# Optimization experiments

Measured on AMD Instinct MI355X. Metric: run time of the kernel, lower is better.

Reference implementation:

```python
import jax, jax.numpy as jnp
import numpy as np

TEMP = 0.07
EPS = 1e-8
NUM_CLASSES = 7
THRESH = 0.3


def setup_inputs() -> dict:
    key = jax.random.key(0)
    k1, k2, k3, k4, k5 = jax.random.split(key, 5)
    N, H, E, C = 8192, 128, 256, NUM_CLASSES
    reps = jax.random.normal(k1, (N, H), dtype=jnp.float32)
    labels = jax.random.randint(k2, (N,), 0, C, dtype=jnp.int64 if jax.config.jax_enable_x64 else jnp.int32)
    centers = jax.random.normal(k3, (C, E), dtype=jnp.float32)
    fc_w = jax.random.normal(k4, (H, E), dtype=jnp.float32) * (1.0 / np.sqrt(E))
    fc_b = jax.random.normal(k5, (H,), dtype=jnp.float32) * 0.01
    return {"reps": reps, "labels": labels, "centers": centers, "fc_w": fc_w, "fc_b": fc_b}


def reference(reps, labels, centers, fc_w, fc_b):
    # fc(default_centers): [C, H]
    curr_centers = centers @ fc_w.T + fc_b
    pad_labels = jnp.arange(NUM_CLASSES, dtype=labels.dtype)

    all_reps = jnp.concatenate([reps, curr_centers], axis=0)      # [M, H]
    all_labels = jnp.concatenate([labels, pad_labels], axis=0)    # [M]
    B = reps.shape[0]
    M = all_reps.shape[0]

    # cosine similarity via normalized matmul (avoids [B,M,H] broadcast)
    norms = jnp.sqrt(jnp.sum(all_reps * all_reps, axis=-1))
    rn = all_reps / jnp.maximum(norms, 1e-8)[:, None]
    cos = rn[:B] @ rn.T                                           # [B, M]

    scores = (1.0 + cos) * 0.5 + EPS
    eye = (jnp.arange(B)[:, None] == jnp.arange(M)[None, :]).astype(scores.dtype)
    scores = scores * (1.0 - eye) / TEMP
    # torch uses .item() on the max -> a non-differentiable constant
    scores = scores - jax.lax.stop_gradient(jnp.max(scores))
    e = jnp.exp(scores)

    pos_mask = (labels[:, None] == all_labels[None, :]).astype(scores.dtype)  # [B, M]
    mask = 1.0 - eye

    pos_sum = jnp.sum(e * pos_mask * mask, axis=-1)
    neg_sum = jnp.sum(e * (1.0 - pos_mask), axis=-1)
    probs = pos_sum / (pos_sum + neg_sum)
    probs = probs / (jnp.sum(pos_mask * mask, axis=-1) + EPS)

    loss_vec = -jnp.log(probs + EPS)
    loss_mask = (loss_vec > THRESH).astype(loss_vec.dtype)
    denom = jax.lax.stop_gradient(jnp.sum(loss_mask)) + EPS
    loss = jnp.sum(loss_vec * loss_mask) / denom
    return loss
```

## Files before the change

### kernel.cpp

```cpp
#include <hip/hip_runtime.h>
#include <hip/hip_bf16.h>

#define BN 8192
#define MM 8199
#define MP 8208
#define HH 128
#define EE 256
#define GX 128
#define GY 16
#define NUM_HIST 7

typedef __attribute__((ext_vector_type(8))) short short8;
typedef __attribute__((ext_vector_type(4))) float floatx4;


__global__ __launch_bounds__(256)
void prep_kernel(const float* __restrict__ reps,
                 const int* __restrict__ labels,
                 const float* __restrict__ centers,
                 const float* __restrict__ fc_w,
                 const float* __restrict__ fc_b,
                 __hip_bfloat16* __restrict__ rnt,
                 int* __restrict__ labp,
                 float* __restrict__ tot) {
  const int wid = threadIdx.x >> 6, lane = threadIdx.x & 63;
  const int b = blockIdx.x;
  if (b < 2048) {
    if (threadIdx.x < 8) tot[b * 8 + threadIdx.x] = 0.f;
    const int r = b * 4 + wid;
    float2 v = ((const float2*)(reps + (size_t)r * HH))[lane];
    float ss = v.x * v.x + v.y * v.y;
#pragma unroll
    for (int m = 1; m < 64; m <<= 1) ss += __shfl_xor(ss, m);
    float inv = 1.0f / fmaxf(sqrtf(ss), 1e-8f);
    __hip_bfloat162 h2;
    h2.x = __float2bfloat16(v.x * inv);
    h2.y = __float2bfloat16(v.y * inv);
    size_t o = (size_t)(r >> 4) * 1024 + (lane >> 2) * 64 + (r & 15) * 4 + (lane & 3);
    ((__hip_bfloat162*)rnt)[o] = h2;
    if (lane == 0) labp[r] = labels[r];
  } else {
    __shared__ float currs[7 * HH];
    for (int o = threadIdx.x; o < 7 * HH; o += 256) {
      int c = o >> 7, h = o & 127;
      const float4* ce = (const float4*)(centers + c * EE);
      const float4* w  = (const float4*)(fc_w + h * EE);
      float s = 0.f;
#pragma unroll 4
      for (int j = 0; j < EE / 4; ++j) {
        float4 a = ce[j], bb = w[j];
        s += a.x * bb.x + a.y * bb.y + a.z * bb.z + a.w * bb.w;
      }
      currs[o] = s + fc_b[h];
    }
    __syncthreads();
    for (int k = 0; k < 4; ++k) {
      int c = wid * 4 + k;
      int r = BN + c;
      float2 v = make_float2(0.f, 0.f);
      if (c < 7) v = ((const float2*)(currs + c * HH))[lane];
      float ss = v.x * v.x + v.y * v.y;
#pragma unroll
      for (int m = 1; m < 64; m <<= 1) ss += __shfl_xor(ss, m);
      float inv = 1.0f / fmaxf(sqrtf(ss), 1e-8f);
      __hip_bfloat162 h2;
      h2.x = __float2bfloat16(v.x * inv);
      h2.y = __float2bfloat16(v.y * inv);
      size_t o = (size_t)(r >> 4) * 1024 + (lane >> 2) * 64 + (r & 15) * 4 + (lane & 3);
      ((__hip_bfloat162*)rnt)[o] = h2;
      if (lane == 0) labp[r] = (r < MM) ? r - BN : -1;
    }
  }
}

__global__ __launch_bounds__(256, 2)
void main_kernel(const __hip_bfloat16* __restrict__ rnt,
                 const int* __restrict__ labp,
                 float* __restrict__ tot,
                 float* __restrict__ pos) {
  __shared__ float red[128];
  const int lane = threadIdx.x & 63;
  const int wid  = threadIdx.x >> 6;
  const int q = lane >> 4, col = lane & 15;
  const int ibase = blockIdx.x * 64;
  const int chunk = (blockIdx.y << 2) | wid;
  const short* rns = (const short*)rnt;

  if (threadIdx.x < 128) red[threadIdx.x] = 0.f;

  short8 afrag[4][4];
#pragma unroll
  for (int it = 0; it < 4; ++it) {
    const short* base = rns + (size_t)(blockIdx.x * 4 + it) * 2048 + lane * 8;
    afrag[it][0] = *(const short8*)(base);
    afrag[it][1] = *(const short8*)(base + 512);
    afrag[it][2] = *(const short8*)(base + 1024);
    afrag[it][3] = *(const short8*)(base + 1536);
  }
  int labi[4][4];
#pragma unroll
  for (int it = 0; it < 4; ++it)
#pragma unroll
    for (int r = 0; r < 4; ++r)
      labi[it][r] = labp[ibase + it * 16 + q * 4 + r];

  float stot[4][4] = {};
  float spos[4][4] = {};
  const float K2 = 10.30496147f;

  const short* bptr = rns + (size_t)chunk * 2048 + lane * 8;
  const int* lptr = labp + chunk * 16 + col;

  for (int jb = chunk * 16; jb < MP; jb += 1024) {
    short8 b0 = *(const short8*)(bptr);
    short8 b1 = *(const short8*)(bptr + 512);
    short8 b2 = *(const short8*)(bptr + 1024);
    short8 b3 = *(const short8*)(bptr + 1536);
    const int labj = *lptr;
    bptr += 64 * 2048;
    lptr += 1024;
#pragma unroll
    for (int it = 0; it < 4; ++it) {
      floatx4 acc = {0.f, 0.f, 0.f, 0.f};
      acc = __builtin_amdgcn_mfma_f32_16x16x32_bf16(afrag[it][0], b0, acc, 0, 0, 0);
      acc = __builtin_amdgcn_mfma_f32_16x16x32_bf16(afrag[it][1], b1, acc, 0, 0, 0);
      acc = __builtin_amdgcn_mfma_f32_16x16x32_bf16(afrag[it][2], b2, acc, 0, 0, 0);
      acc = __builtin_amdgcn_mfma_f32_16x16x32_bf16(afrag[it][3], b3, acc, 0, 0, 0);
      const bool isdiag = (jb == ibase + it * 16);
#pragma unroll
      for (int r = 0; r < 4; ++r) {
        float e = __builtin_amdgcn_exp2f(fmaf(acc[r], K2, -K2));
        if (isdiag && (col == q * 4 + r)) e = 0.f;
        stot[it][r] += e;
        spos[it][r] += (labj == labi[it][r]) ? e : 0.f;
      }
    }
  }

  __syncthreads();

#pragma unroll
  for (int it = 0; it < 4; ++it)
#pragma unroll
    for (int r = 0; r < 4; ++r) {
      float tt = stot[it][r], pp = spos[it][r];
#pragma unroll
      for (int m = 1; m <= 8; m <<= 1) {
        tt += __shfl_xor(tt, m);
        pp += __shfl_xor(pp, m);
      }
      if (col == 0) {
        int li = it * 16 + q * 4 + r;
        atomicAdd(&red[li], tt);
        atomicAdd(&red[64 + li], pp);
      }
    }
  __syncthreads();
  if (threadIdx.x < 64)       atomicAdd(&tot[ibase + threadIdx.x], red[threadIdx.x]);
  else if (threadIdx.x < 128) atomicAdd(&pos[ibase + threadIdx.x - 64], red[threadIdx.x]);
}

__global__ __launch_bounds__(1024)
void loss_kernel(const float* __restrict__ tot,
                 const float* __restrict__ pos,
                 const int* __restrict__ labels,
                 float* __restrict__ out) {
  __shared__ int hist[NUM_HIST];
  __shared__ float s1[16], s2[16];
  const int tid = threadIdx.x;
  const int lane = tid & 63, wid = tid >> 6;
  if (tid < NUM_HIST) hist[tid] = 0;
  __syncthreads();
  int c0 = 0, c1 = 0, c2 = 0, c3 = 0, c4 = 0, c5 = 0, c6 = 0;
  for (int i = tid; i < BN; i += 1024) {
    int lab = labels[i];
    unsigned long long m0 = __ballot(lab == 0);
    unsigned long long m1 = __ballot(lab == 1);
    unsigned long long m2 = __ballot(lab == 2);
    unsigned long long m3 = __ballot(lab == 3);
    unsigned long long m4 = __ballot(lab == 4);
    unsigned long long m5 = __ballot(lab == 5);
    unsigned long long m6 = __ballot(lab == 6);
    if (lane == 0) {
      c0 += __popcll(m0); c1 += __popcll(m1); c2 += __popcll(m2);
      c3 += __popcll(m3); c4 += __popcll(m4); c5 += __popcll(m5);
      c6 += __popcll(m6);
    }
  }
  if (lane == 0) {
    atomicAdd(&hist[0], c0); atomicAdd(&hist[1], c1); atomicAdd(&hist[2], c2);
    atomicAdd(&hist[3], c3); atomicAdd(&hist[4], c4); atomicAdd(&hist[5], c5);
    atomicAdd(&hist[6], c6);
  }
  __syncthreads();
  const float K2 = 10.30496147f;
  const float epad9 = 9.0f * exp2f(-K2);
  float lsum = 0.f, msum = 0.f;
  for (int i = tid; i < BN; i += 1024) {
    float t = tot[i] - epad9;
    float p = pos[i];
    float c = (float)hist[labels[i]];
    float pr = (p / t) / (c + 1e-8f);
    float lv = -logf(pr + 1e-8f);
    if (lv > 0.3f) { lsum += lv; msum += 1.f; }
  }
#pragma unroll
  for (int m = 1; m < 64; m <<= 1) {
    lsum += __shfl_xor(lsum, m);
    msum += __shfl_xor(msum, m);
  }
  if (lane == 0) { s1[wid] = lsum; s2[wid] = msum; }
  __syncthreads();
  if (wid == 0) {
    float a = (lane < 16) ? s1[lane] : 0.f;
    float b = (lane < 16) ? s2[lane] : 0.f;
#pragma unroll
    for (int m = 1; m < 16; m <<= 1) {
      a += __shfl_xor(a, m);
      b += __shfl_xor(b, m);
    }
    if (lane == 0) out[0] = a / (b + 1e-8f);
  }
}

extern "C" void kernel_launch(void* const* d_in, const int* in_sizes, int n_in,
                              void* d_out, int out_size, void* d_ws, size_t ws_size,
                              hipStream_t stream) {
  const float* reps    = (const float*)d_in[0];
  const int*   labels  = (const int*)d_in[1];
  const float* centers = (const float*)d_in[2];
  const float* fc_w    = (const float*)d_in[3];
  const float* fc_b    = (const float*)d_in[4];
  float* out = (float*)d_out;

  char* ws = (char*)d_ws;
  int* labp   = (int*)(ws + 4096);
  __hip_bfloat16* rnt = (__hip_bfloat16*)(ws + 40960);
  float* tot = (float*)(ws + 40960 + 2101248);
  float* pos = tot + BN;

  prep_kernel<<<2049, 256, 0, stream>>>(reps, labels, centers, fc_w, fc_b, rnt, labp, tot);
  main_kernel<<<dim3(GX, GY), 256, 0, stream>>>(rnt, labp, tot, pos);
  loss_kernel<<<1, 1024, 0, stream>>>(tot, pos, labels, out);
}
```

Measured before the change: 143.1 us.

## Share B tiles across waves via double-buffered LDS in similarity kernel

New measurement: 135.4 us. 5.3% less time.

```diff
diff --git a/kernel.cpp b/kernel.cpp
--- a/kernel.cpp
+++ b/kernel.cpp
@@ -6,7 +6,7 @@
 #define MP 8208
 #define HH 128
 #define EE 256
-#define GX 128
+#define GX2 64
 #define GY 16
 #define NUM_HIST 7
 
@@ -78,55 +78,64 @@
                  const int* __restrict__ labp,
                  float* __restrict__ tot,
                  float* __restrict__ pos) {
-  __shared__ float red[128];
+  __shared__ short lbuf[2][2048];
   const int lane = threadIdx.x & 63;
-  const int wid  = threadIdx.x >> 6;
+  const int w    = threadIdx.x >> 6;
   const int q = lane >> 4, col = lane & 15;
-  const int ibase = blockIdx.x * 64;
-  const int chunk = (blockIdx.y << 2) | wid;
+  const int ibase = blockIdx.x * 128;
   const short* rns = (const short*)rnt;
 
-  if (threadIdx.x < 128) red[threadIdx.x] = 0.f;
-
-  short8 afrag[4][4];
-#pragma unroll
-  for (int it = 0; it < 4; ++it) {
-    const short* base = rns + (size_t)(blockIdx.x * 4 + it) * 2048 + lane * 8;
+  short8 afrag[2][4];
+  int tix[2];
+#pragma unroll
+  for (int it = 0; it < 2; ++it) {
+    tix[it] = blockIdx.x * 8 + w * 2 + it;
+    const short* base = rns + (size_t)tix[it] * 2048 + lane * 8;
     afrag[it][0] = *(const short8*)(base);
     afrag[it][1] = *(const short8*)(base + 512);
     afrag[it][2] = *(const short8*)(base + 1024);
     afrag[it][3] = *(const short8*)(base + 1536);
   }
-  int labi[4][4];
-#pragma unroll
-  for (int it = 0; it < 4; ++it)
+  int labi[2][4];
+#pragma unroll
+  for (int it = 0; it < 2; ++it)
 #pragma unroll
     for (int r = 0; r < 4; ++r)
-      labi[it][r] = labp[ibase + it * 16 + q * 4 + r];
-
-  float stot[4][4] = {};
-  float spos[4][4] = {};
+      labi[it][r] = labp[ibase + (w * 2 + it) * 16 + q * 4 + r];
+
+  float stot[2][4] = {};
+  float spos[2][4] = {};
   const float K2 = 10.30496147f;
 
-  const short* bptr = rns + (size_t)chunk * 2048 + lane * 8;
-  const int* lptr = labp + chunk * 16 + col;
-
-  for (int jb = chunk * 16; jb < MP; jb += 1024) {
-    short8 b0 = *(const short8*)(bptr);
-    short8 b1 = *(const short8*)(bptr + 512);
-    short8 b2 = *(const short8*)(bptr + 1024);
-    short8 b3 = *(const short8*)(bptr + 1536);
-    const int labj = *lptr;
-    bptr += 64 * 2048;
-    lptr += 1024;
-#pragma unroll
-    for (int it = 0; it < 4; ++it) {
+  const int t0 = blockIdx.y * 32;
+  const int nt = (blockIdx.y == GY - 1) ? 33 : 32;
+
+  *(short8*)&lbuf[0][threadIdx.x * 8] =
+      *(const short8*)(rns + (size_t)t0 * 2048 + threadIdx.x * 8);
+  __syncthreads();
+
+  for (int s = 0; s < nt; ++s) {
+    const int cur = s & 1;
+    const int t = t0 + s;
+    if (s + 1 < nt)
+      *(short8*)&lbuf[cur ^ 1][threadIdx.x * 8] =
+          *(const short8*)(rns + (size_t)(t + 1) * 2048 + threadIdx.x * 8);
+
+    const short* lb = &lbuf[cur][0];
+    short8 b0 = *(const short8*)(lb + lane * 8);
+    short8 b1 = *(const short8*)(lb + 512 + lane * 8);
+    short8 b2 = *(const short8*)(lb + 1024 + lane * 8);
+    short8 b3 = *(const short8*)(lb + 1536 + lane * 8);
+    const int labj = labp[t * 16 + col];
+
+#pragma unroll
+    for (int it = 0; it < 2; ++it) {
       floatx4 acc = {0.f, 0.f, 0.f, 0.f};
       acc = __builtin_amdgcn_mfma_f32_16x16x32_bf16(afrag[it][0], b0, acc, 0, 0, 0);
       acc = __builtin_amdgcn_mfma_f32_16x16x32_bf16(afrag[it][1], b1, acc, 0, 0, 0);
       acc = __builtin_amdgcn_mfma_f32_16x16x32_bf16(afrag[it][2], b2, acc, 0, 0, 0);
       acc = __builtin_amdgcn_mfma_f32_16x16x32_bf16(afrag[it][3], b3, acc, 0, 0, 0);
-      const bool isdiag = (jb == ibase + it * 16);
+      const bool isdiag = (t == tix[it]);
 #pragma unroll
       for (int r = 0; r < 4; ++r) {
         float e = __builtin_amdgcn_exp2f(fmaf(acc[r], K2, -K2));
@@ -135,12 +144,11 @@
         spos[it][r] += (labj == labi[it][r]) ? e : 0.f;
       }
     }
-  }
-
-  __syncthreads();
-
-#pragma unroll
-  for (int it = 0; it < 4; ++it)
+    __syncthreads();
+  }
+
+#pragma unroll
+  for (int it = 0; it < 2; ++it)
 #pragma unroll
     for (int r = 0; r < 4; ++r) {
       float tt = stot[it][r], pp = spos[it][r];
@@ -150,14 +158,11 @@
         pp += __shfl_xor(pp, m);
       }
       if (col == 0) {
-        int li = it * 16 + q * 4 + r;
-        atomicAdd(&red[li], tt);
-        atomicAdd(&red[64 + li], pp);
-      }
-    }
-  __syncthreads();
-  if (threadIdx.x < 64)       atomicAdd(&tot[ibase + threadIdx.x], red[threadIdx.x]);
-  else if (threadIdx.x < 128) atomicAdd(&pos[ibase + threadIdx.x - 64], red[threadIdx.x]);
+        int i = ibase + (w * 2 + it) * 16 + q * 4 + r;
+        atomicAdd(&tot[i], tt);
+        atomicAdd(&pos[i], pp);
+      }
+    }
 }
 
 __global__ __launch_bounds__(1024)
@@ -240,6 +245,6 @@
   float* pos = tot + BN;
 
   prep_kernel<<<2049, 256, 0, stream>>>(reps, labels, centers, fc_w, fc_b, rnt, labp, tot);
-  main_kernel<<<dim3(GX, GY), 256, 0, stream>>>(rnt, labp, tot, pos);
+  main_kernel<<<dim3(GX2, GY), 256, 0, stream>>>(rnt, labp, tot, pos);
   loss_kernel<<<1, 1024, 0, stream>>>(tot, pos, labels, out);
 }
```
